# Kernel optimization log

Measured on AMD Instinct MI355X. Metric: run time of the kernel, lower is better.

The kernel has to match this reference:

```python
import jax, jax.numpy as jnp
import numpy as np

NUM_NODES_GLOBAL = 100000
EMBED_DIM = 256
NUM_RELATIONS = 16
N_LOCAL = 16384
N_EDGES = 131072
N_QUERIES = 4096


def setup_inputs() -> dict:
    key = jax.random.key(0)
    ks = jax.random.split(key, 12)
    node_emb = jax.random.normal(ks[0], (NUM_NODES_GLOBAL, EMBED_DIM), dtype=jnp.float32)
    # RGCN layer 1 params: per-relation weight (R, in, out), root weight, bias
    w1 = jax.random.normal(ks[1], (NUM_RELATIONS, EMBED_DIM, EMBED_DIM), dtype=jnp.float32) * 0.05
    root1 = jax.random.normal(ks[2], (EMBED_DIM, EMBED_DIM), dtype=jnp.float32) * 0.05
    b1 = jnp.zeros((EMBED_DIM,), dtype=jnp.float32)
    w2 = jax.random.normal(ks[3], (NUM_RELATIONS, EMBED_DIM, EMBED_DIM), dtype=jnp.float32) * 0.05
    root2 = jax.random.normal(ks[4], (EMBED_DIM, EMBED_DIM), dtype=jnp.float32) * 0.05
    b2 = jnp.zeros((EMBED_DIM,), dtype=jnp.float32)
    edge_index = jax.random.randint(ks[5], (2, N_EDGES), 0, N_LOCAL, dtype=jnp.int64)
    edge_type = jax.random.randint(ks[6], (N_EDGES,), 0, NUM_RELATIONS, dtype=jnp.int64)
    entity_ids = jax.random.randint(ks[7], (N_LOCAL,), 0, NUM_NODES_GLOBAL, dtype=jnp.int64)
    batch_ids = jnp.sort(jax.random.randint(ks[8], (N_LOCAL,), 0, N_QUERIES, dtype=jnp.int64))
    return {"node_emb": node_emb, "w1": w1, "root1": root1, "b1": b1,
            "w2": w2, "root2": root2, "b2": b2,
            "edge_index": edge_index, "edge_type": edge_type,
            "entity_ids": entity_ids, "batch_ids": batch_ids}


def rgcn_layer(x, W, Wroot, b, src, tgt, edge_type, num_relations):
    """PyG RGCNConv (num_bases=None, aggr='mean', root_weight=True, bias=True).

    out[i] = sum_r mean_{j: (j -r-> i)} x_j @ W[r]  +  x_i @ Wroot + b
    Aggregation done per (target, relation) bucket, then a single (N,R,d)x(R,d,d) einsum.
    """
    n = x.shape[0]
    d = x.shape[1]
    bucket = tgt * num_relations + edge_type  # (E,) combined (node, relation) key
    ones = jnp.ones(src.shape, dtype=x.dtype)
    cnt = jax.ops.segment_sum(ones, bucket, num_segments=n * num_relations)
    agg = jax.ops.segment_sum(x[src], bucket, num_segments=n * num_relations)
    agg = agg.reshape(n, num_relations, d) / jnp.maximum(cnt, 1.0).reshape(n, num_relations, 1)
    return jnp.einsum('nrd,rdo->no', agg, W) + x @ Wroot + b


def reference(node_emb, w1, root1, b1, w2, root2, b2, edge_index, edge_type, entity_ids, batch_ids):
    x = node_emb[entity_ids]                      # (N_local, d) gather from global table
    src, tgt = edge_index[0], edge_index[1]
    x = rgcn_layer(x, w1, root1, b1, src, tgt, edge_type, NUM_RELATIONS)
    x = rgcn_layer(x, w2, root2, b2, src, tgt, edge_type, NUM_RELATIONS)
    # scatter-sum readout per query
    return jax.ops.segment_sum(x, batch_ids, num_segments=N_QUERIES)
```

## Files before the change

### kernel.cpp

```cpp
#include <hip/hip_runtime.h>
#include <hip/hip_bf16.h>

#define NLOCAL 16384
#define NEDGES 131072
#define NREL   16
#define DIM    256
#define NQ     4096
#define NBLKS  512
#define NSLOTS (NEDGES + NREL * 64)

typedef __bf16 bf16x8 __attribute__((ext_vector_type(8)));
typedef float  f32x4  __attribute__((ext_vector_type(4)));
typedef unsigned short u16x4 __attribute__((ext_vector_type(4)));
typedef unsigned short u16x8 __attribute__((ext_vector_type(8)));

static __device__ __forceinline__ unsigned short f2bf(float f) {
    union { float f; unsigned u; } v; v.f = f;
    unsigned r = v.u + 0x7FFFu + ((v.u >> 16) & 1u);
    return (unsigned short)(r >> 16);
}
static __device__ __forceinline__ float bf2f(unsigned short s) {
    union { unsigned u; float f; } v; v.u = ((unsigned)s) << 16;
    return v.f;
}

__global__ void k_gather(const float* __restrict__ emb, const int* __restrict__ ids,
                         unsigned short* __restrict__ x0) {
    int gid = blockIdx.x * blockDim.x + threadIdx.x;
    int i = gid >> 5, c8 = gid & 31;
    int e = ids[i];
    const f32x4* src = (const f32x4*)(emb + (size_t)e * DIM + c8 * 8);
    f32x4 a = src[0], b = src[1];
    u16x8 u;
    u[0] = f2bf(a[0]); u[1] = f2bf(a[1]); u[2] = f2bf(a[2]); u[3] = f2bf(a[3]);
    u[4] = f2bf(b[0]); u[5] = f2bf(b[1]); u[6] = f2bf(b[2]); u[7] = f2bf(b[3]);
    *(u16x8*)&x0[(size_t)i * DIM + c8 * 8] = u;
}

__global__ void k_transpose_all(const float* __restrict__ w1, const float* __restrict__ r1,
                                const float* __restrict__ w2, const float* __restrict__ r2,
                                unsigned short* __restrict__ WT1, unsigned short* __restrict__ rT1,
                                unsigned short* __restrict__ WT2, unsigned short* __restrict__ rT2) {
    __shared__ float t[64][65];
    int blk = blockIdx.x;
    const float* W; unsigned short* WT; int tr;
    if (blk < 256)      { W = w1 + (size_t)(blk >> 4) * DIM * DIM; WT = WT1 + (size_t)(blk >> 4) * DIM * DIM; tr = blk & 15; }
    else if (blk < 272) { W = r1; WT = rT1; tr = blk - 256; }
    else if (blk < 528) { int q = blk - 272; W = w2 + (size_t)(q >> 4) * DIM * DIM; WT = WT2 + (size_t)(q >> 4) * DIM * DIM; tr = q & 15; }
    else                { W = r2; WT = rT2; tr = blk - 528; }
    int tk = (tr >> 2) << 6;
    int to = (tr & 3) << 6;
    #pragma unroll
    for (int it = 0; it < 16; ++it) {
        int el = it * 256 + threadIdx.x;
        int row = el >> 6, col = el & 63;
        t[row][col] = W[(size_t)(tk + row) * DIM + to + col];
    }
    __syncthreads();
    #pragma unroll
    for (int it = 0; it < 16; ++it) {
        int el = it * 256 + threadIdx.x;
        int row = el >> 6, col = el & 63;
        WT[(size_t)(to + row) * DIM + tk + col] = f2bf(t[col][row]);
    }
}

__global__ void k_hist2(const int* __restrict__ eidx, const int* __restrict__ etype,
                        unsigned int* __restrict__ cnt, unsigned int* __restrict__ cnt_t,
                        int* __restrict__ bh) {
    __shared__ int h[NREL];
    int tid = threadIdx.x;
    if (tid < NREL) h[tid] = 0;
    __syncthreads();
    int e = blockIdx.x * 256 + tid;
    int rel = etype[e];
    int tgt = eidx[NEDGES + e];
    atomicAdd(&cnt[tgt * NREL + rel], 1u);
    atomicAdd(&cnt_t[tgt], 1u);
    atomicAdd(&h[rel], 1);
    __syncthreads();
    if (tid < NREL) bh[tid * NBLKS + blockIdx.x] = h[tid];
}

__global__ void k_scan_par(int* __restrict__ bh, int* __restrict__ meta) {
    __shared__ int tot[NREL];
    __shared__ int base[NREL];
    int w = threadIdx.x >> 6, lane = threadIdx.x & 63;
    int vals[8];
    int run = 0;
    #pragma unroll
    for (int c = 0; c < 8; ++c) {
        int v = bh[w * NBLKS + c * 64 + lane];
        int s = v;
        #pragma unroll
        for (int off = 1; off < 64; off <<= 1) {
            int t = __shfl_up(s, off);
            if (lane >= off) s += t;
        }
        vals[c] = run + s - v;
        run += __shfl(s, 63);
    }
    if (lane == 0) tot[w] = run;
    __syncthreads();
    if (threadIdx.x == 0) {
        int s = 0;
        for (int r = 0; r < NREL; ++r) { base[r] = s; meta[16 + r] = s; s += (tot[r] + 63) & ~63; }
        meta[32] = s;
    }
    __syncthreads();
    int b = base[w];
    #pragma unroll
    for (int c = 0; c < 8; ++c) bh[w * NBLKS + c * 64 + lane] = vals[c] + b;
}

__global__ void k_place2(const int* __restrict__ eidx, const int* __restrict__ etype,
                         const int* __restrict__ bh, int* __restrict__ ssrc,
                         int* __restrict__ stgt) {
    __shared__ int cur[NREL];
    int tid = threadIdx.x;
    if (tid < NREL) cur[tid] = bh[tid * NBLKS + blockIdx.x];
    __syncthreads();
    int e = blockIdx.x * 256 + tid;
    int rel = etype[e];
    int pos = atomicAdd(&cur[rel], 1);
    ssrc[pos] = eidx[e];
    stgt[pos] = eidx[NEDGES + e];
}

__global__ void k_scan_t(const unsigned int* __restrict__ cnt_t, int* __restrict__ row_ptr,
                         int* __restrict__ cur) {
    __shared__ int wsum[16];
    int tid = threadIdx.x;
    int wave = tid >> 6, lane = tid & 63;
    int base = tid * 16;
    int loc[16];
    int s = 0;
    #pragma unroll
    for (int c = 0; c < 16; ++c) { loc[c] = s; s += (int)cnt_t[base + c]; }
    int inc = s;
    #pragma unroll
    for (int off = 1; off < 64; off <<= 1) {
        int t = __shfl_up(inc, off);
        if (lane >= off) inc += t;
    }
    if (lane == 63) wsum[wave] = inc;
    __syncthreads();
    if (tid == 0) {
        int a = 0;
        for (int w = 0; w < 16; ++w) { int v = wsum[w]; wsum[w] = a; a += v; }
    }
    __syncthreads();
    int excl = wsum[wave] + inc - s;
    #pragma unroll
    for (int c = 0; c < 16; ++c) { int v = excl + loc[c]; row_ptr[base + c] = v; cur[base + c] = v; }
    if (tid == 1023) row_ptr[NLOCAL] = excl + s;
}

__global__ void k_place_t(const int* __restrict__ ssrc, const int* __restrict__ stgt,
                          int* __restrict__ cur, int* __restrict__ elist) {
    int p = blockIdx.x * 256 + threadIdx.x;
    int s = ssrc[p];
    if (s >= 0) {
        int tgt = stgt[p];
        int pos = atomicAdd(&cur[tgt], 1);
        elist[pos] = p;
    }
}

#define AS_IDX(row, c16) ((row) * 64 + (((c16) ^ ((row) & 7)) << 3))

__launch_bounds__(256)
__global__ void k_gemm_root(const unsigned short* __restrict__ X, const unsigned short* __restrict__ BT,
                            const float* __restrict__ bias, unsigned short* __restrict__ Y) {
    __shared__ __align__(16) unsigned short As[2][64 * 64];
    int tid = threadIdx.x;
    int wave = tid >> 6, lane = tid & 63;
    int l16 = lane & 15, grp = lane >> 4;
    int bm = blockIdx.x;
    int arow = tid >> 3, ac16 = tid & 7;

    f32x4 acc[4][4];
    #pragma unroll
    for (int i = 0; i < 4; ++i)
        #pragma unroll
        for (int j = 0; j < 4; ++j) acc[i][j] = f32x4{0.f, 0.f, 0.f, 0.f};

    #pragma unroll
    for (int it = 0; it < 2; ++it) {
        int row = it * 32 + arow;
        u16x8 u = *(const u16x8*)&X[(size_t)(bm * 64 + row) * DIM + ac16 * 8];
        *(u16x8*)&As[0][AS_IDX(row, ac16)] = u;
    }
    for (int kt = 0; kt < 4; ++kt) {
        __syncthreads();
        if (kt < 3) {
            #pragma unroll
            for (int it = 0; it < 2; ++it) {
                int row = it * 32 + arow;
                u16x8 u = *(const u16x8*)&X[(size_t)(bm * 64 + row) * DIM + (kt + 1) * 64 + ac16 * 8];
                *(u16x8*)&As[(kt + 1) & 1][AS_IDX(row, ac16)] = u;
            }
        }
        const unsigned short* buf = As[kt & 1];
        #pragma unroll
        for (int kk = 0; kk < 2; ++kk) {
            bf16x8 a[4], b[4];
            #pragma unroll
            for (int i = 0; i < 4; ++i)
                a[i] = *(const bf16x8*)&buf[AS_IDX(i * 16 + l16, kk * 4 + grp)];
            #pragma unroll
            for (int j = 0; j < 4; ++j)
                b[j] = *(const bf16x8*)&BT[(size_t)(wave * 64 + j * 16 + l16) * DIM + kt * 64 + kk * 32 + grp * 8];
            #pragma unroll
            for (int i = 0; i < 4; ++i)
                #pragma unroll
                for (int j = 0; j < 4; ++j)
                    acc[i][j] = __builtin_amdgcn_mfma_f32_16x16x32_bf16(a[i], b[j], acc[i][j], 0, 0, 0);
        }
    }
    #pragma unroll
    for (int i = 0; i < 4; ++i)
        #pragma unroll
        for (int reg = 0; reg < 4; ++reg) {
            int row = i * 16 + grp * 4 + reg;
            int gr = bm * 64 + row;
            #pragma unroll
            for (int j = 0; j < 4; ++j) {
                int col = wave * 64 + j * 16 + l16;
                float v = acc[i][j][reg] + bias[col];
                float vo = __shfl_xor(v, 1);
                if (!(lane & 1)) {
                    unsigned pk = (unsigned)f2bf(v) | ((unsigned)f2bf(vo) << 16);
                    *(unsigned*)&Y[(size_t)gr * DIM + col] = pk;
                }
            }
        }
}

__launch_bounds__(256)
__global__ void k_gemm_edge(const unsigned short* __restrict__ X, const unsigned short* __restrict__ WT,
                            const int* __restrict__ ssrc, const int* __restrict__ stgt,
                            const unsigned int* __restrict__ cnt, const int* __restrict__ meta,
                            unsigned short* __restrict__ ye) {
    int base = blockIdx.x * 64;
    if (base >= meta[32]) return;
    int rel = 0;
    while (rel < 15 && meta[16 + rel + 1] <= base) ++rel;
    const unsigned short* BT = WT + (size_t)rel * DIM * DIM;

    __shared__ __align__(16) unsigned short As[2][64 * 64];
    int tid = threadIdx.x;
    int wave = tid >> 6, lane = tid & 63;
    int l16 = lane & 15, grp = lane >> 4;
    int arow = tid >> 3, ac16 = tid & 7;

    f32x4 acc[4][4];
    #pragma unroll
    for (int i = 0; i < 4; ++i)
        #pragma unroll
        for (int j = 0; j < 4; ++j) acc[i][j] = f32x4{0.f, 0.f, 0.f, 0.f};

    int s0 = ssrc[base + arow];
    int s1 = ssrc[base + 32 + arow];
    #pragma unroll
    for (int it = 0; it < 2; ++it) {
        int row = it * 32 + arow;
        int s = it ? s1 : s0;
        u16x8 u = {};
        if (s >= 0) u = *(const u16x8*)&X[(size_t)s * DIM + ac16 * 8];
        *(u16x8*)&As[0][AS_IDX(row, ac16)] = u;
    }
    for (int kt = 0; kt < 4; ++kt) {
        __syncthreads();
        if (kt < 3) {
            #pragma unroll
            for (int it = 0; it < 2; ++it) {
                int row = it * 32 + arow;
                int s = it ? s1 : s0;
                u16x8 u = {};
                if (s >= 0) u = *(const u16x8*)&X[(size_t)s * DIM + (kt + 1) * 64 + ac16 * 8];
                *(u16x8*)&As[(kt + 1) & 1][AS_IDX(row, ac16)] = u;
            }
        }
        const unsigned short* buf = As[kt & 1];
        #pragma unroll
        for (int kk = 0; kk < 2; ++kk) {
            bf16x8 a[4], b[4];
            #pragma unroll
            for (int i = 0; i < 4; ++i)
                a[i] = *(const bf16x8*)&buf[AS_IDX(i * 16 + l16, kk * 4 + grp)];
            #pragma unroll
            for (int j = 0; j < 4; ++j)
                b[j] = *(const bf16x8*)&BT[(size_t)(wave * 64 + j * 16 + l16) * DIM + kt * 64 + kk * 32 + grp * 8];
            #pragma unroll
            for (int i = 0; i < 4; ++i)
                #pragma unroll
                for (int j = 0; j < 4; ++j)
                    acc[i][j] = __builtin_amdgcn_mfma_f32_16x16x32_bf16(a[i], b[j], acc[i][j], 0, 0, 0);
        }
    }
    #pragma unroll
    for (int i = 0; i < 4; ++i)
        #pragma unroll
        for (int reg = 0; reg < 4; ++reg) {
            int row = i * 16 + grp * 4 + reg;
            int e = base + row;
            int s = ssrc[e];
            int tgt = stgt[e];
            float rc = (s >= 0) ? 1.0f / fmaxf((float)cnt[tgt * NREL + rel], 1.0f) : 0.0f;
            #pragma unroll
            for (int j = 0; j < 4; ++j) {
                int col = wave * 64 + j * 16 + l16;
                float v = acc[i][j][reg] * rc;
                float vo = __shfl_xor(v, 1);
                if (s >= 0 && !(lane & 1)) {
                    unsigned pk = (unsigned)f2bf(v) | ((unsigned)f2bf(vo) << 16);
                    *(unsigned*)&ye[(size_t)e * DIM + col] = pk;
                }
            }
        }
}

__global__ void k_combine(const unsigned short* __restrict__ rootY, const unsigned short* __restrict__ ye,
                          const int* __restrict__ row_ptr, const int* __restrict__ elist,
                          unsigned short* __restrict__ Xout) {
    int wave = threadIdx.x >> 6, lane = threadIdx.x & 63;
    int tgt = blockIdx.x * 4 + wave;
    int c0 = lane * 4;
    u16x4 rv = *(const u16x4*)&rootY[(size_t)tgt * DIM + c0];
    float a0 = bf2f(rv[0]), a1 = bf2f(rv[1]), a2 = bf2f(rv[2]), a3 = bf2f(rv[3]);
    int p0 = row_ptr[tgt], p1 = row_ptr[tgt + 1];
    for (int p = p0; p < p1; ++p) {
        int idx = elist[p];
        u16x4 v = *(const u16x4*)&ye[(size_t)idx * DIM + c0];
        a0 += bf2f(v[0]); a1 += bf2f(v[1]); a2 += bf2f(v[2]); a3 += bf2f(v[3]);
    }
    u16x4 o;
    o[0] = f2bf(a0); o[1] = f2bf(a1); o[2] = f2bf(a2); o[3] = f2bf(a3);
    *(u16x4*)&Xout[(size_t)tgt * DIM + c0] = o;
}

__global__ void k_readout(const unsigned short* __restrict__ X2, const int* __restrict__ bids,
                          float* __restrict__ out) {
    int gid = blockIdx.x * blockDim.x + threadIdx.x;
    int g = gid >> 5, c8 = gid & 31;
    int i0 = g * 8;
    float a[8];
    #pragma unroll
    for (int j = 0; j < 8; ++j) a[j] = 0.f;
    int curq = bids[i0];
    #pragma unroll
    for (int t = 0; t < 8; ++t) {
        int i = i0 + t;
        int q = bids[i];
        if (q != curq) {
            #pragma unroll
            for (int j = 0; j < 8; ++j) {
                unsafeAtomicAdd(&out[(size_t)curq * DIM + c8 * 8 + j], a[j]);
                a[j] = 0.f;
            }
            curq = q;
        }
        u16x8 v = *(const u16x8*)&X2[(size_t)i * DIM + c8 * 8];
        #pragma unroll
        for (int j = 0; j < 8; ++j) a[j] += bf2f(v[j]);
    }
    #pragma unroll
    for (int j = 0; j < 8; ++j)
        unsafeAtomicAdd(&out[(size_t)curq * DIM + c8 * 8 + j], a[j]);
}

extern "C" void kernel_launch(void* const* d_in, const int* in_sizes, int n_in,
                              void* d_out, int out_size, void* d_ws, size_t ws_size,
                              hipStream_t stream) {
    const float* emb   = (const float*)d_in[0];
    const float* w1    = (const float*)d_in[1];
    const float* root1 = (const float*)d_in[2];
    const float* b1    = (const float*)d_in[3];
    const float* w2    = (const float*)d_in[4];
    const float* root2 = (const float*)d_in[5];
    const float* b2    = (const float*)d_in[6];
    const int* eidx    = (const int*)d_in[7];
    const int* etype   = (const int*)d_in[8];
    const int* eids    = (const int*)d_in[9];
    const int* bids    = (const int*)d_in[10];
    float* out = (float*)d_out;

    char* ws = (char*)d_ws;
    unsigned short* x0   = (unsigned short*)(ws + (size_t)(0 << 20));
    unsigned short* x1   = (unsigned short*)(ws + (size_t)(8 << 20));
    unsigned short* x2   = (unsigned short*)(ws + (size_t)(16 << 20));
    unsigned short* WT1  = (unsigned short*)(ws + (size_t)(24 << 20));
    unsigned short* rT1  = (unsigned short*)(ws + (size_t)(26 << 20));
    unsigned short* WT2  = (unsigned short*)(ws + (size_t)(27 << 20));
    unsigned short* rT2  = (unsigned short*)(ws + (size_t)(29 << 20));
    unsigned int*   cnt  = (unsigned int*)(ws + (size_t)(30 << 20));
    int*           meta  = (int*)(ws + (size_t)(31 << 20));
    int*           ssrc  = (int*)(ws + (size_t)(31 << 20) + 4096);
    int*           stgt  = (int*)(ws + (size_t)(32 << 20));
    int*           bh    = (int*)(ws + (size_t)(33 << 20));
    unsigned int*  cnt_t = (unsigned int*)(ws + (size_t)(33 << 20) + 65536);
    int*         row_ptr = (int*)(ws + (size_t)(33 << 20) + 2 * 65536);
    int*           cur_t = (int*)(ws + (size_t)(33 << 20) + 3 * 65536 + 4096);
    int*           elist = (int*)(ws + (size_t)(34 << 20));
    unsigned short* rootY= (unsigned short*)(ws + (size_t)(35 << 20));
    unsigned short* ye   = (unsigned short*)(ws + (size_t)(43 << 20));

    const int NBLK_EDGE = NSLOTS / 64;

    hipMemsetAsync(cnt, 0, (size_t)NLOCAL * NREL * 4, stream);
    hipMemsetAsync(cnt_t, 0, (size_t)NLOCAL * 4, stream);
    hipMemsetAsync(ssrc, 0xFF, (size_t)NSLOTS * 4, stream);
    hipMemsetAsync(out, 0, (size_t)NQ * DIM * 4, stream);

    k_gather<<<2048, 256, 0, stream>>>(emb, eids, x0);
    k_transpose_all<<<544, 256, 0, stream>>>(w1, root1, w2, root2, WT1, rT1, WT2, rT2);
    k_hist2<<<NBLKS, 256, 0, stream>>>(eidx, etype, cnt, cnt_t, bh);
    k_scan_par<<<1, 1024, 0, stream>>>(bh, meta);
    k_place2<<<NBLKS, 256, 0, stream>>>(eidx, etype, bh, ssrc, stgt);
    k_scan_t<<<1, 1024, 0, stream>>>(cnt_t, row_ptr, cur_t);
    k_place_t<<<NSLOTS / 256, 256, 0, stream>>>(ssrc, stgt, cur_t, elist);

    k_gemm_root<<<NLOCAL / 64, 256, 0, stream>>>(x0, rT1, b1, rootY);
    k_gemm_edge<<<NBLK_EDGE, 256, 0, stream>>>(x0, WT1, ssrc, stgt, cnt, meta, ye);
    k_combine<<<NLOCAL / 4, 256, 0, stream>>>(rootY, ye, row_ptr, elist, x1);
    k_gemm_root<<<NLOCAL / 64, 256, 0, stream>>>(x1, rT2, b2, rootY);
    k_gemm_edge<<<NBLK_EDGE, 256, 0, stream>>>(x1, WT2, ssrc, stgt, cnt, meta, ye);
    k_combine<<<NLOCAL / 4, 256, 0, stream>>>(rootY, ye, row_ptr, elist, x2);

    k_readout<<<256, 256, 0, stream>>>(x2, bids, out);
}
```

Before: 470.2 us.

## Merge scan kernels, fuse target placement, stage GEMM epilogues through LDS

The relation scan and the target CSR scan are merged into one kernel, and per-target edge-list placement now happens inside the relation placement kernel, which drops two launches and a pass over the slot array. A per-block relation table is precomputed so edge GEMM blocks no longer search meta. Both GEMMs hoist their B-fragment loads ahead of the MFMA loop and stage bf16 outputs in shared memory to emit coalesced 16-byte row stores instead of scattered 4-byte ones. The cost is 32KB of LDS per block, which may lower occupancy, plus extra barriers. Edge-list order inside each target now depends on atomic timing, so bf16 summation order can vary between runs.

```diff
diff --git a/kernel.cpp b/kernel.cpp
--- a/kernel.cpp
+++ b/kernel.cpp
@@ -8,6 +8,7 @@
 #define NQ     4096
 #define NBLKS  512
 #define NSLOTS (NEDGES + NREL * 64)
+#define NBLKE  (NSLOTS / 64)
 
 typedef __bf16 bf16x8 __attribute__((ext_vector_type(8)));
 typedef float  f32x4  __attribute__((ext_vector_type(4)));
@@ -82,10 +83,15 @@
     if (tid < NREL) bh[tid * NBLKS + blockIdx.x] = h[tid];
 }
 
-__global__ void k_scan_par(int* __restrict__ bh, int* __restrict__ meta) {
+__global__ void k_scan_all(int* __restrict__ bh, int* __restrict__ meta,
+                           const unsigned int* __restrict__ cnt_t, int* __restrict__ row_ptr,
+                           int* __restrict__ cur_t, int* __restrict__ blk_rel) {
     __shared__ int tot[NREL];
-    __shared__ int base[NREL];
-    int w = threadIdx.x >> 6, lane = threadIdx.x & 63;
+    __shared__ int rs[NREL + 1];
+    __shared__ int wsum[16];
+    int tid = threadIdx.x;
+    int w = tid >> 6, lane = tid & 63;
+
     int vals[8];
     int run = 0;
     #pragma unroll
@@ -102,69 +108,65 @@
     }
     if (lane == 0) tot[w] = run;
     __syncthreads();
-    if (threadIdx.x == 0) {
+    if (tid == 0) {
         int s = 0;
-        for (int r = 0; r < NREL; ++r) { base[r] = s; meta[16 + r] = s; s += (tot[r] + 63) & ~63; }
-        meta[32] = s;
-    }
-    __syncthreads();
-    int b = base[w];
-    #pragma unroll
-    for (int c = 0; c < 8; ++c) bh[w * NBLKS + c * 64 + lane] = vals[c] + b;
+        for (int r = 0; r < NREL; ++r) { rs[r] = s; meta[16 + r] = s; s += (tot[r] + 63) & ~63; }
+        rs[NREL] = s; meta[32] = s;
+    }
+    __syncthreads();
+    int b0 = rs[w];
+    #pragma unroll
+    for (int c = 0; c < 8; ++c) bh[w * NBLKS + c * 64 + lane] = vals[c] + b0;
+
+    int total = rs[NREL];
+    for (int b = tid; b < NBLKE; b += 1024) {
+        int base = b * 64;
+        int r;
+        if (base >= total) r = -1;
+        else { r = 0; while (r < 15 && rs[r + 1] <= base) ++r; }
+        blk_rel[b] = r;
+    }
+
+    int base16 = tid * 16;
+    int loc[16];
+    int s = 0;
+    #pragma unroll
+    for (int c = 0; c < 16; ++c) { loc[c] = s; s += (int)cnt_t[base16 + c]; }
+    int inc = s;
+    #pragma unroll
+    for (int off = 1; off < 64; off <<= 1) {
+        int t = __shfl_up(inc, off);
+        if (lane >= off) inc += t;
+    }
+    if (lane == 63) wsum[w] = inc;
+    __syncthreads();
+    if (tid == 0) {
+        int a = 0;
+        for (int q = 0; q < 16; ++q) { int v = wsum[q]; wsum[q] = a; a += v; }
+    }
+    __syncthreads();
+    int excl = wsum[w] + inc - s;
+    #pragma unroll
+    for (int c = 0; c < 16; ++c) { int v = excl + loc[c]; row_ptr[base16 + c] = v; cur_t[base16 + c] = v; }
+    if (tid == 1023) row_ptr[NLOCAL] = excl + s;
 }
 
 __global__ void k_place2(const int* __restrict__ eidx, const int* __restrict__ etype,
                          const int* __restrict__ bh, int* __restrict__ ssrc,
-                         int* __restrict__ stgt) {
+                         int* __restrict__ stgt, int* __restrict__ cur_t,
+                         int* __restrict__ elist) {
     __shared__ int cur[NREL];
     int tid = threadIdx.x;
     if (tid < NREL) cur[tid] = bh[tid * NBLKS + blockIdx.x];
     __syncthreads();
     int e = blockIdx.x * 256 + tid;
     int rel = etype[e];
+    int tgt = eidx[NEDGES + e];
     int pos = atomicAdd(&cur[rel], 1);
     ssrc[pos] = eidx[e];
-    stgt[pos] = eidx[NEDGES + e];
-}
-
-__global__ void k_scan_t(const unsigned int* __restrict__ cnt_t, int* __restrict__ row_ptr,
-                         int* __restrict__ cur) {
-    __shared__ int wsum[16];
-    int tid = threadIdx.x;
-    int wave = tid >> 6, lane = tid & 63;
-    int base = tid * 16;
-    int loc[16];
-    int s = 0;
-    #pragma unroll
-    for (int c = 0; c < 16; ++c) { loc[c] = s; s += (int)cnt_t[base + c]; }
-    int inc = s;
-    #pragma unroll
-    for (int off = 1; off < 64; off <<= 1) {
-        int t = __shfl_up(inc, off);
-        if (lane >= off) inc += t;
-    }
-    if (lane == 63) wsum[wave] = inc;
-    __syncthreads();
-    if (tid == 0) {
-        int a = 0;
-        for (int w = 0; w < 16; ++w) { int v = wsum[w]; wsum[w] = a; a += v; }
-    }
-    __syncthreads();
-    int excl = wsum[wave] + inc - s;
-    #pragma unroll
-    for (int c = 0; c < 16; ++c) { int v = excl + loc[c]; row_ptr[base + c] = v; cur[base + c] = v; }
-    if (tid == 1023) row_ptr[NLOCAL] = excl + s;
-}
-
-__global__ void k_place_t(const int* __restrict__ ssrc, const int* __restrict__ stgt,
-                          int* __restrict__ cur, int* __restrict__ elist) {
-    int p = blockIdx.x * 256 + threadIdx.x;
-    int s = ssrc[p];
-    if (s >= 0) {
-        int tgt = stgt[p];
-        int pos = atomicAdd(&cur[tgt], 1);
-        elist[pos] = p;
-    }
+    stgt[pos] = tgt;
+    int q = atomicAdd(&cur_t[tgt], 1);
+    elist[q] = pos;
 }
 
 #define AS_IDX(row, c16) ((row) * 64 + (((c16) ^ ((row) & 7)) << 3))
@@ -172,7 +174,9 @@
 __launch_bounds__(256)
 __global__ void k_gemm_root(const unsigned short* __restrict__ X, const unsigned short* __restrict__ BT,
                             const float* __restrict__ bias, unsigned short* __restrict__ Y) {
-    __shared__ __align__(16) unsigned short As[2][64 * 64];
+    __shared__ __align__(16) unsigned short smem[16384];
+    unsigned short* As0 = smem;
+    unsigned short* As1 = smem + 4096;
     int tid = threadIdx.x;
     int wave = tid >> 6, lane = tid & 63;
     int l16 = lane & 15, grp = lane >> 4;
@@ -189,41 +193,45 @@
     for (int it = 0; it < 2; ++it) {
         int row = it * 32 + arow;
         u16x8 u = *(const u16x8*)&X[(size_t)(bm * 64 + row) * DIM + ac16 * 8];
-        *(u16x8*)&As[0][AS_IDX(row, ac16)] = u;
+        *(u16x8*)&As0[AS_IDX(row, ac16)] = u;
     }
     for (int kt = 0; kt < 4; ++kt) {
         __syncthreads();
         if (kt < 3) {
+            unsigned short* dst = (kt & 1) ? As0 : As1;
             #pragma unroll
             for (int it = 0; it < 2; ++it) {
                 int row = it * 32 + arow;
                 u16x8 u = *(const u16x8*)&X[(size_t)(bm * 64 + row) * DIM + (kt + 1) * 64 + ac16 * 8];
-                *(u16x8*)&As[(kt + 1) & 1][AS_IDX(row, ac16)] = u;
+                *(u16x8*)&dst[AS_IDX(row, ac16)] = u;
             }
         }
-        const unsigned short* buf = As[kt & 1];
+        const unsigned short* buf = (kt & 1) ? As1 : As0;
+        bf16x8 b[2][4];
+        #pragma unroll
+        for (int kk = 0; kk < 2; ++kk)
+            #pragma unroll
+            for (int j = 0; j < 4; ++j)
+                b[kk][j] = *(const bf16x8*)&BT[(size_t)(wave * 64 + j * 16 + l16) * DIM + kt * 64 + kk * 32 + grp * 8];
         #pragma unroll
         for (int kk = 0; kk < 2; ++kk) {
-            bf16x8 a[4], b[4];
+            bf16x8 a[4];
             #pragma unroll
             for (int i = 0; i < 4; ++i)
                 a[i] = *(const bf16x8*)&buf[AS_IDX(i * 16 + l16, kk * 4 + grp)];
-            #pragma unroll
-            for (int j = 0; j < 4; ++j)
-                b[j] = *(const bf16x8*)&BT[(size_t)(wave * 64 + j * 16 + l16) * DIM + kt * 64 + kk * 32 + grp * 8];
             #pragma unroll
             for (int i = 0; i < 4; ++i)
                 #pragma unroll
                 for (int j = 0; j < 4; ++j)
-                    acc[i][j] = __builtin_amdgcn_mfma_f32_16x16x32_bf16(a[i], b[j], acc[i][j], 0, 0, 0);
-        }
-    }
+                    acc[i][j] = __builtin_amdgcn_mfma_f32_16x16x32_bf16(a[i], b[kk][j], acc[i][j], 0, 0, 0);
+        }
+    }
+    __syncthreads();
     #pragma unroll
     for (int i = 0; i < 4; ++i)
         #pragma unroll
         for (int reg = 0; reg < 4; ++reg) {
             int row = i * 16 + grp * 4 + reg;
-            int gr = bm * 64 + row;
             #pragma unroll
             for (int j = 0; j < 4; ++j) {
                 int col = wave * 64 + j * 16 + l16;
@@ -231,24 +239,33 @@
                 float vo = __shfl_xor(v, 1);
                 if (!(lane & 1)) {
                     unsigned pk = (unsigned)f2bf(v) | ((unsigned)f2bf(vo) << 16);
-                    *(unsigned*)&Y[(size_t)gr * DIM + col] = pk;
+                    *(unsigned*)&smem[row * 256 + col] = pk;
                 }
             }
         }
+    __syncthreads();
+    int r = tid >> 2;
+    size_t orow = (size_t)(bm * 64 + r) * DIM;
+    #pragma unroll
+    for (int it = 0; it < 8; ++it) {
+        int ch = (tid & 3) + it * 4;
+        *(u16x8*)&Y[orow + ch * 8] = *(const u16x8*)&smem[r * 256 + ch * 8];
+    }
 }
 
 __launch_bounds__(256)
 __global__ void k_gemm_edge(const unsigned short* __restrict__ X, const unsigned short* __restrict__ WT,
                             const int* __restrict__ ssrc, const int* __restrict__ stgt,
-                            const unsigned int* __restrict__ cnt, const int* __restrict__ meta,
+                            const unsigned int* __restrict__ cnt, const int* __restrict__ blk_rel,
                             unsigned short* __restrict__ ye) {
+    int rel = blk_rel[blockIdx.x];
+    if (rel < 0) return;
     int base = blockIdx.x * 64;
-    if (base >= meta[32]) return;
-    int rel = 0;
-    while (rel < 15 && meta[16 + rel + 1] <= base) ++rel;
     const unsigned short* BT = WT + (size_t)rel * DIM * DIM;
 
-    __shared__ __align__(16) unsigned short As[2][64 * 64];
+    __shared__ __align__(16) unsigned short smem[16384];
+    unsigned short* As0 = smem;
+    unsigned short* As1 = smem + 4096;
     int tid = threadIdx.x;
     int wave = tid >> 6, lane = tid & 63;
     int l16 = lane & 15, grp = lane >> 4;
@@ -268,37 +285,42 @@
         int s = it ? s1 : s0;
         u16x8 u = {};
         if (s >= 0) u = *(const u16x8*)&X[(size_t)s * DIM + ac16 * 8];
-        *(u16x8*)&As[0][AS_IDX(row, ac16)] = u;
+        *(u16x8*)&As0[AS_IDX(row, ac16)] = u;
     }
     for (int kt = 0; kt < 4; ++kt) {
         __syncthreads();
         if (kt < 3) {
+            unsigned short* dst = (kt & 1) ? As0 : As1;
             #pragma unroll
             for (int it = 0; it < 2; ++it) {
                 int row = it * 32 + arow;
                 int s = it ? s1 : s0;
                 u16x8 u = {};
                 if (s >= 0) u = *(const u16x8*)&X[(size_t)s * DIM + (kt + 1) * 64 + ac16 * 8];
-                *(u16x8*)&As[(kt + 1) & 1][AS_IDX(row, ac16)] = u;
+                *(u16x8*)&dst[AS_IDX(row, ac16)] = u;
             }
         }
-        const unsigned short* buf = As[kt & 1];
+        const unsigned short* buf = (kt & 1) ? As1 : As0;
+        bf16x8 b[2][4];
+        #pragma unroll
+        for (int kk = 0; kk < 2; ++kk)
+            #pragma unroll
+            for (int j = 0; j < 4; ++j)
+                b[kk][j] = *(const bf16x8*)&BT[(size_t)(wave * 64 + j * 16 + l16) * DIM + kt * 64 + kk * 32 + grp * 8];
         #pragma unroll
         for (int kk = 0; kk < 2; ++kk) {
-            bf16x8 a[4], b[4];
+            bf16x8 a[4];
             #pragma unroll
             for (int i = 0; i < 4; ++i)
                 a[i] = *(const bf16x8*)&buf[AS_IDX(i * 16 + l16, kk * 4 + grp)];
-            #pragma unroll
-            for (int j = 0; j < 4; ++j)
-                b[j] = *(const bf16x8*)&BT[(size_t)(wave * 64 + j * 16 + l16) * DIM + kt * 64 + kk * 32 + grp * 8];
             #pragma unroll
             for (int i = 0; i < 4; ++i)
                 #pragma unroll
                 for (int j = 0; j < 4; ++j)
-                    acc[i][j] = __builtin_amdgcn_mfma_f32_16x16x32_bf16(a[i], b[j], acc[i][j], 0, 0, 0);
-        }
-    }
+                    acc[i][j] = __builtin_amdgcn_mfma_f32_16x16x32_bf16(a[i], b[kk][j], acc[i][j], 0, 0, 0);
+        }
+    }
+    __syncthreads();
     #pragma unroll
     for (int i = 0; i < 4; ++i)
         #pragma unroll
@@ -313,12 +335,22 @@
                 int col = wave * 64 + j * 16 + l16;
                 float v = acc[i][j][reg] * rc;
                 float vo = __shfl_xor(v, 1);
-                if (s >= 0 && !(lane & 1)) {
+                if (!(lane & 1)) {
                     unsigned pk = (unsigned)f2bf(v) | ((unsigned)f2bf(vo) << 16);
-                    *(unsigned*)&ye[(size_t)e * DIM + col] = pk;
+                    *(unsigned*)&smem[row * 256 + col] = pk;
                 }
             }
         }
+    __syncthreads();
+    int r = tid >> 2;
+    if (ssrc[base + r] >= 0) {
+        size_t orow = (size_t)(base + r) * DIM;
+        #pragma unroll
+        for (int it = 0; it < 8; ++it) {
+            int ch = (tid & 3) + it * 4;
+            *(u16x8*)&ye[orow + ch * 8] = *(const u16x8*)&smem[r * 256 + ch * 8];
+        }
+    }
 }
 
 __global__ void k_combine(const unsigned short* __restrict__ rootY, const unsigned short* __restrict__ ye,
@@ -401,12 +433,11 @@
     int*           bh    = (int*)(ws + (size_t)(33 << 20));
     unsigned int*  cnt_t = (unsigned int*)(ws + (size_t)(33 << 20) + 65536);
     int*         row_ptr = (int*)(ws + (size_t)(33 << 20) + 2 * 65536);
-    int*           cur_t = (int*)(ws + (size_t)(33 << 20) + 3 * 65536 + 4096);
+    int*           cur_t = (int*)(ws + (size_t)(33 << 20) + 4 * 65536);
+    int*         blk_rel = (int*)(ws + (size_t)(33 << 20) + 6 * 65536);
     int*           elist = (int*)(ws + (size_t)(34 << 20));
     unsigned short* rootY= (unsigned short*)(ws + (size_t)(35 << 20));
     unsigned short* ye   = (unsigned short*)(ws + (size_t)(43 << 20));
-
-    const int NBLK_EDGE = NSLOTS / 64;
 
     hipMemsetAsync(cnt, 0, (size_t)NLOCAL * NREL * 4, stream);
     hipMemsetAsync(cnt_t, 0, (size_t)NLOCAL * 4, stream);
@@ -416,16 +447,14 @@
     k_gather<<<2048, 256, 0, stream>>>(emb, eids, x0);
     k_transpose_all<<<544, 256, 0, stream>>>(w1, root1, w2, root2, WT1, rT1, WT2, rT2);
     k_hist2<<<NBLKS, 256, 0, stream>>>(eidx, etype, cnt, cnt_t, bh);
-    k_scan_par<<<1, 1024, 0, stream>>>(bh, meta);
-    k_place2<<<NBLKS, 256, 0, stream>>>(eidx, etype, bh, ssrc, stgt);
-    k_scan_t<<<1, 1024, 0, stream>>>(cnt_t, row_ptr, cur_t);
-    k_place_t<<<NSLOTS / 256, 256, 0, stream>>>(ssrc, stgt, cur_t, elist);
+    k_scan_all<<<1, 1024, 0, stream>>>(bh, meta, cnt_t, row_ptr, cur_t, blk_rel);
+    k_place2<<<NBLKS, 256, 0, stream>>>(eidx, etype, bh, ssrc, stgt, cur_t, elist);
 
     k_gemm_root<<<NLOCAL / 64, 256, 0, stream>>>(x0, rT1, b1, rootY);
-    k_gemm_edge<<<NBLK_EDGE, 256, 0, stream>>>(x0, WT1, ssrc, stgt, cnt, meta, ye);
+    k_gemm_edge<<<NBLKE, 256, 0, stream>>>(x0, WT1, ssrc, stgt, cnt, blk_rel, ye);
     k_combine<<<NLOCAL / 4, 256, 0, stream>>>(rootY, ye, row_ptr, elist, x1);
     k_gemm_root<<<NLOCAL / 64, 256, 0, stream>>>(x1, rT2, b2, rootY);
-    k_gemm_edge<<<NBLK_EDGE, 256, 0, stream>>>(x1, WT2, ssrc, stgt, cnt, meta, ye);
+    k_gemm_edge<<<NBLKE, 256, 0, stream>>>(x1, WT2, ssrc, stgt, cnt, blk_rel, ye);
     k_combine<<<NLOCAL / 4, 256, 0, stream>>>(rootY, ye, row_ptr, elist, x2);
 
     k_readout<<<256, 256, 0, stream>>>(x2, bids, out);
```

Measured after the change: 468.0 us. About the same (-0.5%).
